# Performance work log

Measured on AMD Instinct MI355X. Metric: run time of the kernel, lower is better.

The kernel has to match this reference:

```python
import jax, jax.numpy as jnp
import numpy as np
from jax import lax


def setup_inputs() -> dict:
    key = jax.random.key(0)
    k1, k2, k3 = jax.random.split(key, 3)
    B, T, dimIn, dimH = 64, 2048, 128, 256
    x = jax.random.normal(k1, (B, T, dimIn), dtype=jnp.float32)
    h = jnp.zeros((B, dimH), dtype=jnp.float32)
    # torch nn.Linear(dimIn+dimH, dimH): weight [dimH, dimIn+dimH], bias [dimH]
    fan_in = dimIn + dimH
    bound = 1.0 / np.sqrt(fan_in)
    W = jax.random.uniform(k2, (dimH, fan_in), minval=-bound, maxval=bound, dtype=jnp.float32)
    b = jax.random.uniform(k3, (dimH,), minval=-bound, maxval=bound, dtype=jnp.float32)
    return {"x": x, "h": h, "W": W, "b": b}


def reference(x, h, W, b):
    # x: [B, T, dimIn], h: [B, H], W: [H, dimIn+H], b: [H]
    dimIn = x.shape[-1]
    Wx = W[:, :dimIn]   # [H, dimIn] -- acts on x part of concat
    Wh = W[:, dimIn:]   # [H, H]     -- acts on h part of concat
    # Precompute the input projection for all timesteps in one GEMM.
    xw = jnp.einsum('btd,hd->bth', x, Wx) + b  # [B, T, H]

    def step(h_prev, xw_t):
        h_new = jnp.tanh(xw_t + h_prev @ Wh.T)  # tanh(Linear(cat(x,h)))
        return h_new, h_new

    _, res = lax.scan(step, h, jnp.swapaxes(xw, 0, 1))  # res: [T, B, H]
    return jnp.swapaxes(res, 0, 1)  # [B, T, H]
```

## Files before the change

kernel.cpp:

```cpp
#include <hip/hip_runtime.h>
#include <hip/hip_fp16.h>

#define TSEQ  2048
#define BATCH 64
#define DIN   128
#define DH    256
#define WSTR  384
#define NCH   (TSEQ / 16)

typedef __fp16 h2    __attribute__((ext_vector_type(2)));
typedef __fp16 f16x8 __attribute__((ext_vector_type(8)));
typedef float  f32x4 __attribute__((ext_vector_type(4)));

static __device__ __forceinline__ h2 bc_h2(unsigned int u) {
    return __builtin_bit_cast(h2, u);
}

#define DPP_XOR1(v) __builtin_bit_cast(float, \
    __builtin_amdgcn_mov_dpp(__builtin_bit_cast(int, (v)), 0xB1, 0xF, 0xF, true))
#define DPP_XOR2(v) __builtin_bit_cast(float, \
    __builtin_amdgcn_mov_dpp(__builtin_bit_cast(int, (v)), 0x4E, 0xF, 0xF, true))
#define DPP_XOR8(v) __builtin_bit_cast(float, \
    __builtin_amdgcn_mov_dpp(__builtin_bit_cast(int, (v)), 0x128, 0xF, 0xF, true))

__global__ __launch_bounds__(256) void xw_gemm(const float* __restrict__ x,
                                               const float* __restrict__ W,
                                               const float* __restrict__ bias,
                                               float* __restrict__ out) {
    __shared__ __align__(16) __fp16 af[64][136];

    const int tid  = threadIdx.x;
    const int lane = tid & 63;
    const int wv   = tid >> 6;
    const int row0 = blockIdx.x * 64;
    const int nlo  = lane & 15;
    const int quad = lane >> 4;

    {
        const int r  = tid >> 2;
        const int c0 = (tid & 3) * 32;
        const float4* xr = (const float4*)(x + (size_t)(row0 + r) * DIN) + (tid & 3) * 8;
#pragma unroll
        for (int i = 0; i < 4; ++i) {
            float4 f0 = xr[2 * i];
            float4 f1 = xr[2 * i + 1];
            f16x8 v;
            v[0]=(__fp16)f0.x; v[1]=(__fp16)f0.y; v[2]=(__fp16)f0.z; v[3]=(__fp16)f0.w;
            v[4]=(__fp16)f1.x; v[5]=(__fp16)f1.y; v[6]=(__fp16)f1.z; v[7]=(__fp16)f1.w;
            *(f16x8*)&af[r][c0 + i * 8] = v;
        }
    }

    f16x8 bfr[4][4];
#pragma unroll
    for (int n0 = 0; n0 < 4; ++n0) {
        const int n = wv * 64 + n0 * 16 + nlo;
        const float* wr = W + (size_t)n * WSTR;
#pragma unroll
        for (int kk = 0; kk < 4; ++kk) {
            const int k = kk * 32 + quad * 8;
            float4 f0 = *(const float4*)(wr + k);
            float4 f1 = *(const float4*)(wr + k + 4);
            f16x8 v;
            v[0]=(__fp16)f0.x; v[1]=(__fp16)f0.y; v[2]=(__fp16)f0.z; v[3]=(__fp16)f0.w;
            v[4]=(__fp16)f1.x; v[5]=(__fp16)f1.y; v[6]=(__fp16)f1.z; v[7]=(__fp16)f1.w;
            bfr[n0][kk] = v;
        }
    }
    __syncthreads();

    f32x4 acc[4][4];
#pragma unroll
    for (int m0 = 0; m0 < 4; ++m0)
#pragma unroll
        for (int n0 = 0; n0 < 4; ++n0) acc[m0][n0] = (f32x4)0.0f;

#pragma unroll
    for (int kk = 0; kk < 4; ++kk) {
#pragma unroll
        for (int m0 = 0; m0 < 4; ++m0) {
            f16x8 a = *(const f16x8*)&af[m0 * 16 + nlo][kk * 32 + quad * 8];
#pragma unroll
            for (int n0 = 0; n0 < 4; ++n0)
                acc[m0][n0] = __builtin_amdgcn_mfma_f32_16x16x32_f16(
                                  a, bfr[n0][kk], acc[m0][n0], 0, 0, 0);
        }
    }

#pragma unroll
    for (int n0 = 0; n0 < 4; ++n0) {
        const int col = wv * 64 + n0 * 16 + nlo;
        const float bn = bias[col];
#pragma unroll
        for (int m0 = 0; m0 < 4; ++m0)
#pragma unroll
            for (int r = 0; r < 4; ++r) {
                const int row = row0 + m0 * 16 + quad * 4 + r;
                out[(size_t)row * DH + col] = acc[m0][n0][r] + bn;
            }
    }
}

__global__ __launch_bounds__(256, 1) void rnn_scan(const float* __restrict__ W,
                                                   const float* __restrict__ h0,
                                                   float* __restrict__ out) {
    __shared__ __align__(16) __fp16 hseg[2][8][40];

    const int tid = threadIdx.x;
    const int b   = blockIdx.x;
    const int sig = (tid & 3) | ((tid & 8) >> 1);

    h2 w[8][16];
#pragma unroll
    for (int r = 0; r < 8; ++r) {
        const int rho = (r & 3) | ((r & 4) << 1);
        const float* wr = W + (size_t)(tid ^ rho) * WSTR + DIN + 32 * sig;
#pragma unroll
        for (int j = 0; j < 8; ++j) {
            float4 f = *(const float4*)(wr + 4 * j);
            w[r][2 * j]     = h2{(__fp16)f.x, (__fp16)f.y};
            w[r][2 * j + 1] = h2{(__fp16)f.z, (__fp16)f.w};
        }
    }
#pragma unroll
    for (int r = 0; r < 8; ++r)
#pragma unroll
        for (int i = 0; i < 16; ++i)
            asm volatile("" : "+v"(w[r][i]));

    hseg[0][tid >> 5][tid & 31] = (__fp16)h0[(size_t)b * DH + tid];

    const float* gsrc = out + (size_t)b * TSEQ * DH + tid;
    float*       gdst = out + (size_t)b * TSEQ * DH + tid;

    float xwreg[16];
#pragma unroll
    for (int s = 0; s < 16; ++s) xwreg[s] = gsrc[(size_t)s * DH];

    asm volatile("s_waitcnt lgkmcnt(0)\n\ts_barrier" ::: "memory");

#pragma unroll 1
    for (int c = 0; c < NCH; ++c) {
        const float* gnext = gsrc + (size_t)(c + 1 < NCH ? c + 1 : 0) * (16 * DH);
        float*       gout  = gdst + (size_t)c * (16 * DH);

#pragma unroll
        for (int s = 0; s < 16; ++s) {
            const float xw_s = xwreg[s];
            xwreg[s] = gnext[(size_t)s * DH];
            const int p = s & 1;
            const uint4* hp = (const uint4*)&hseg[p][sig][0];

            float P[8];
#pragma unroll
            for (int r = 0; r < 8; ++r) P[r] = 0.f;
#pragma unroll
            for (int i4 = 0; i4 < 4; ++i4) {
                uint4 v = hp[i4];
                h2 ha = bc_h2(v.x), hb = bc_h2(v.y), hc = bc_h2(v.z), hd = bc_h2(v.w);
#pragma unroll
                for (int r = 0; r < 8; ++r) {
                    P[r] = __builtin_amdgcn_fdot2(w[r][4*i4+0], ha, P[r], false);
                    P[r] = __builtin_amdgcn_fdot2(w[r][4*i4+1], hb, P[r], false);
                    P[r] = __builtin_amdgcn_fdot2(w[r][4*i4+2], hc, P[r], false);
                    P[r] = __builtin_amdgcn_fdot2(w[r][4*i4+3], hd, P[r], false);
                }
            }

            float S0 = P[0] + DPP_XOR1(P[1]);
            float S1 = P[2] + DPP_XOR1(P[3]);
            float S2 = P[4] + DPP_XOR1(P[5]);
            float S3 = P[6] + DPP_XOR1(P[7]);
            float T0 = S0 + DPP_XOR2(S1);
            float T1 = S2 + DPP_XOR2(S3);
            float dot = T0 + DPP_XOR8(T1);

            float pre = xw_s + dot;
            float e  = __expf(2.0f * pre);
            float hn = 1.0f - 2.0f * __builtin_amdgcn_rcpf(e + 1.0f);

            hseg[p ^ 1][tid >> 5][tid & 31] = (__fp16)hn;
            gout[(size_t)s * DH] = hn;

            asm volatile("s_waitcnt lgkmcnt(0)\n\ts_barrier" ::: "memory");
        }
    }
}

extern "C" void kernel_launch(void* const* d_in, const int* in_sizes, int n_in,
                              void* d_out, int out_size, void* d_ws, size_t ws_size,
                              hipStream_t stream) {
    const float* x    = (const float*)d_in[0];
    const float* h0   = (const float*)d_in[1];
    const float* W    = (const float*)d_in[2];
    const float* bias = (const float*)d_in[3];
    float* out = (float*)d_out;

    xw_gemm<<<BATCH * TSEQ / 64, 256, 0, stream>>>(x, W, bias, out);
    rnn_scan<<<BATCH, 256, 0, stream>>>(W, h0, out);
}
```

Measured before the change: 994.7 us.

## Fuse input projection GEMM into RNN scan and split recurrence over 512 threads

Removes the separate xw GEMM kernel and computes each 16-step chunk of the input projection inside the scan block with MFMA, double-buffered in shared memory and overlapped with the recurrence. Doubles threads per block to 512 so each thread handles half the hidden-state dot product, combining the two halves with a ds_bpermute across lanes 32 apart. This avoids writing xw to global memory and reading it back, and shortens each thread's serial dot-product chain. In exchange each step gains an extra cross-lane reduction and half the threads idle during tanh, and the per-chunk GEMM sits on the scan's critical path.

```diff
diff --git a/kernel.cpp b/kernel.cpp
--- a/kernel.cpp
+++ b/kernel.cpp
@@ -23,100 +23,38 @@
 #define DPP_XOR8(v) __builtin_bit_cast(float, \
     __builtin_amdgcn_mov_dpp(__builtin_bit_cast(int, (v)), 0x128, 0xF, 0xF, true))
 
-__global__ __launch_bounds__(256) void xw_gemm(const float* __restrict__ x,
-                                               const float* __restrict__ W,
-                                               const float* __restrict__ bias,
-                                               float* __restrict__ out) {
-    __shared__ __align__(16) __fp16 af[64][136];
+static __device__ __forceinline__ float pair_sum32(float u, int lane) {
+    const int addr = (lane ^ 32) << 2;
+    float v = __builtin_bit_cast(float,
+        __builtin_amdgcn_ds_bpermute(addr, __builtin_bit_cast(int, u)));
+    return u + v;
+}
+
+__global__ __launch_bounds__(512) void rnn_fused(const float* __restrict__ x,
+                                                 const float* __restrict__ W,
+                                                 const float* __restrict__ bias,
+                                                 const float* __restrict__ h0,
+                                                 float* __restrict__ out) {
+    __shared__ __align__(16) __fp16 hseg[2][16][24];
+    __shared__ __align__(16) float  xwb[2][16][DH];
 
     const int tid  = threadIdx.x;
+    const int b    = blockIdx.x;
     const int lane = tid & 63;
     const int wv   = tid >> 6;
-    const int row0 = blockIdx.x * 64;
     const int nlo  = lane & 15;
     const int quad = lane >> 4;
 
-    {
-        const int r  = tid >> 2;
-        const int c0 = (tid & 3) * 32;
-        const float4* xr = (const float4*)(x + (size_t)(row0 + r) * DIN) + (tid & 3) * 8;
-#pragma unroll
-        for (int i = 0; i < 4; ++i) {
-            float4 f0 = xr[2 * i];
-            float4 f1 = xr[2 * i + 1];
-            f16x8 v;
-            v[0]=(__fp16)f0.x; v[1]=(__fp16)f0.y; v[2]=(__fp16)f0.z; v[3]=(__fp16)f0.w;
-            v[4]=(__fp16)f1.x; v[5]=(__fp16)f1.y; v[6]=(__fp16)f1.z; v[7]=(__fp16)f1.w;
-            *(f16x8*)&af[r][c0 + i * 8] = v;
-        }
-    }
+    const int o   = (tid & 31) | ((tid >> 1) & 224);
+    const int sig = (tid & 3) | ((tid & 8) >> 1) | ((tid & 32) >> 2);
 
-    f16x8 bfr[4][4];
-#pragma unroll
-    for (int n0 = 0; n0 < 4; ++n0) {
-        const int n = wv * 64 + n0 * 16 + nlo;
-        const float* wr = W + (size_t)n * WSTR;
-#pragma unroll
-        for (int kk = 0; kk < 4; ++kk) {
-            const int k = kk * 32 + quad * 8;
-            float4 f0 = *(const float4*)(wr + k);
-            float4 f1 = *(const float4*)(wr + k + 4);
-            f16x8 v;
-            v[0]=(__fp16)f0.x; v[1]=(__fp16)f0.y; v[2]=(__fp16)f0.z; v[3]=(__fp16)f0.w;
-            v[4]=(__fp16)f1.x; v[5]=(__fp16)f1.y; v[6]=(__fp16)f1.z; v[7]=(__fp16)f1.w;
-            bfr[n0][kk] = v;
-        }
-    }
-    __syncthreads();
-
-    f32x4 acc[4][4];
-#pragma unroll
-    for (int m0 = 0; m0 < 4; ++m0)
-#pragma unroll
-        for (int n0 = 0; n0 < 4; ++n0) acc[m0][n0] = (f32x4)0.0f;
-
-#pragma unroll
-    for (int kk = 0; kk < 4; ++kk) {
-#pragma unroll
-        for (int m0 = 0; m0 < 4; ++m0) {
-            f16x8 a = *(const f16x8*)&af[m0 * 16 + nlo][kk * 32 + quad * 8];
-#pragma unroll
-            for (int n0 = 0; n0 < 4; ++n0)
-                acc[m0][n0] = __builtin_amdgcn_mfma_f32_16x16x32_f16(
-                                  a, bfr[n0][kk], acc[m0][n0], 0, 0, 0);
-        }
-    }
-
-#pragma unroll
-    for (int n0 = 0; n0 < 4; ++n0) {
-        const int col = wv * 64 + n0 * 16 + nlo;
-        const float bn = bias[col];
-#pragma unroll
-        for (int m0 = 0; m0 < 4; ++m0)
-#pragma unroll
-            for (int r = 0; r < 4; ++r) {
-                const int row = row0 + m0 * 16 + quad * 4 + r;
-                out[(size_t)row * DH + col] = acc[m0][n0][r] + bn;
-            }
-    }
-}
-
-__global__ __launch_bounds__(256, 1) void rnn_scan(const float* __restrict__ W,
-                                                   const float* __restrict__ h0,
-                                                   float* __restrict__ out) {
-    __shared__ __align__(16) __fp16 hseg[2][8][40];
-
-    const int tid = threadIdx.x;
-    const int b   = blockIdx.x;
-    const int sig = (tid & 3) | ((tid & 8) >> 1);
-
-    h2 w[8][16];
+    h2 w[8][8];
 #pragma unroll
     for (int r = 0; r < 8; ++r) {
         const int rho = (r & 3) | ((r & 4) << 1);
-        const float* wr = W + (size_t)(tid ^ rho) * WSTR + DIN + 32 * sig;
+        const float* wr = W + (size_t)(o ^ rho) * WSTR + DIN + 16 * sig;
 #pragma unroll
-        for (int j = 0; j < 8; ++j) {
+        for (int j = 0; j < 4; ++j) {
             float4 f = *(const float4*)(wr + 4 * j);
             w[r][2 * j]     = h2{(__fp16)f.x, (__fp16)f.y};
             w[r][2 * j + 1] = h2{(__fp16)f.z, (__fp16)f.w};
@@ -125,46 +63,97 @@
 #pragma unroll
     for (int r = 0; r < 8; ++r)
 #pragma unroll
-        for (int i = 0; i < 16; ++i)
+        for (int i = 0; i < 8; ++i)
             asm volatile("" : "+v"(w[r][i]));
 
-    hseg[0][tid >> 5][tid & 31] = (__fp16)h0[(size_t)b * DH + tid];
+    f16x8 bfr[2][4];
+#pragma unroll
+    for (int n0 = 0; n0 < 2; ++n0) {
+        const float* wr = W + (size_t)(32 * wv + 16 * n0 + nlo) * WSTR;
+#pragma unroll
+        for (int kk = 0; kk < 4; ++kk) {
+            float4 f0 = *(const float4*)(wr + kk * 32 + quad * 8);
+            float4 f1 = *(const float4*)(wr + kk * 32 + quad * 8 + 4);
+            f16x8 v;
+            v[0]=(__fp16)f0.x; v[1]=(__fp16)f0.y; v[2]=(__fp16)f0.z; v[3]=(__fp16)f0.w;
+            v[4]=(__fp16)f1.x; v[5]=(__fp16)f1.y; v[6]=(__fp16)f1.z; v[7]=(__fp16)f1.w;
+            bfr[n0][kk] = v;
+        }
+    }
+    const float bias0 = bias[32 * wv + nlo];
+    const float bias1 = bias[32 * wv + 16 + nlo];
 
-    const float* gsrc = out + (size_t)b * TSEQ * DH + tid;
-    float*       gdst = out + (size_t)b * TSEQ * DH + tid;
+    const float* xb = x + (size_t)b * TSEQ * DIN;
+    float4 xr[8];
 
-    float xwreg[16];
-#pragma unroll
-    for (int s = 0; s < 16; ++s) xwreg[s] = gsrc[(size_t)s * DH];
+#define LOAD_X(c)                                                            \
+    {                                                                        \
+        const float* xp = xb + (size_t)(16 * (c) + nlo) * DIN;               \
+        _Pragma("unroll")                                                    \
+        for (int kk = 0; kk < 4; ++kk) {                                     \
+            xr[2 * kk]     = *(const float4*)(xp + kk * 32 + quad * 8);      \
+            xr[2 * kk + 1] = *(const float4*)(xp + kk * 32 + quad * 8 + 4);  \
+        }                                                                    \
+    }
 
-    asm volatile("s_waitcnt lgkmcnt(0)\n\ts_barrier" ::: "memory");
+#define MAKE_XW(buf)                                                         \
+    {                                                                        \
+        f32x4 a0 = (f32x4)0.0f, a1 = (f32x4)0.0f;                            \
+        _Pragma("unroll")                                                    \
+        for (int kk = 0; kk < 4; ++kk) {                                     \
+            float4 f0 = xr[2 * kk], f1 = xr[2 * kk + 1];                     \
+            f16x8 a;                                                         \
+            a[0]=(__fp16)f0.x; a[1]=(__fp16)f0.y; a[2]=(__fp16)f0.z;         \
+            a[3]=(__fp16)f0.w; a[4]=(__fp16)f1.x; a[5]=(__fp16)f1.y;         \
+            a[6]=(__fp16)f1.z; a[7]=(__fp16)f1.w;                            \
+            a0 = __builtin_amdgcn_mfma_f32_16x16x32_f16(a, bfr[0][kk], a0, 0, 0, 0); \
+            a1 = __builtin_amdgcn_mfma_f32_16x16x32_f16(a, bfr[1][kk], a1, 0, 0, 0); \
+        }                                                                    \
+        _Pragma("unroll")                                                    \
+        for (int r = 0; r < 4; ++r) {                                        \
+            xwb[buf][quad * 4 + r][32 * wv + nlo]      = a0[r] + bias0;      \
+            xwb[buf][quad * 4 + r][32 * wv + 16 + nlo] = a1[r] + bias1;      \
+        }                                                                    \
+    }
+
+    if (tid < DH) hseg[0][tid >> 4][tid & 15] = (__fp16)h0[(size_t)b * DH + tid];
+
+    LOAD_X(0);
+    MAKE_XW(0);
+    LOAD_X(1);
+    __syncthreads();
+
+    float* orow = out + (size_t)b * TSEQ * DH + o;
 
 #pragma unroll 1
     for (int c = 0; c < NCH; ++c) {
-        const float* gnext = gsrc + (size_t)(c + 1 < NCH ? c + 1 : 0) * (16 * DH);
-        float*       gout  = gdst + (size_t)c * (16 * DH);
+        if (c + 1 < NCH) {
+            MAKE_XW((c + 1) & 1);
+            LOAD_X(c + 2 < NCH ? c + 2 : 0);
+        }
+        const float* xwr = &xwb[c & 1][0][0];
+        float* oc = orow + (size_t)(16 * c) * DH;
 
 #pragma unroll
         for (int s = 0; s < 16; ++s) {
-            const float xw_s = xwreg[s];
-            xwreg[s] = gnext[(size_t)s * DH];
+            const float xw_s = xwr[s * DH + o];
             const int p = s & 1;
             const uint4* hp = (const uint4*)&hseg[p][sig][0];
+            uint4 v0 = hp[0], v1 = hp[1];
+            h2 ha = bc_h2(v0.x), hb = bc_h2(v0.y), hc = bc_h2(v0.z), hd = bc_h2(v0.w);
+            h2 he = bc_h2(v1.x), hf = bc_h2(v1.y), hg = bc_h2(v1.z), hh = bc_h2(v1.w);
 
             float P[8];
 #pragma unroll
-            for (int r = 0; r < 8; ++r) P[r] = 0.f;
-#pragma unroll
-            for (int i4 = 0; i4 < 4; ++i4) {
-                uint4 v = hp[i4];
-                h2 ha = bc_h2(v.x), hb = bc_h2(v.y), hc = bc_h2(v.z), hd = bc_h2(v.w);
-#pragma unroll
-                for (int r = 0; r < 8; ++r) {
-                    P[r] = __builtin_amdgcn_fdot2(w[r][4*i4+0], ha, P[r], false);
-                    P[r] = __builtin_amdgcn_fdot2(w[r][4*i4+1], hb, P[r], false);
-                    P[r] = __builtin_amdgcn_fdot2(w[r][4*i4+2], hc, P[r], false);
-                    P[r] = __builtin_amdgcn_fdot2(w[r][4*i4+3], hd, P[r], false);
-                }
+            for (int r = 0; r < 8; ++r) {
+                P[r] = __builtin_amdgcn_fdot2(w[r][0], ha, 0.0f, false);
+                P[r] = __builtin_amdgcn_fdot2(w[r][1], hb, P[r], false);
+                P[r] = __builtin_amdgcn_fdot2(w[r][2], hc, P[r], false);
+                P[r] = __builtin_amdgcn_fdot2(w[r][3], hd, P[r], false);
+                P[r] = __builtin_amdgcn_fdot2(w[r][4], he, P[r], false);
+                P[r] = __builtin_amdgcn_fdot2(w[r][5], hf, P[r], false);
+                P[r] = __builtin_amdgcn_fdot2(w[r][6], hg, P[r], false);
+                P[r] = __builtin_amdgcn_fdot2(w[r][7], hh, P[r], false);
             }
 
             float S0 = P[0] + DPP_XOR1(P[1]);
@@ -173,18 +162,21 @@
             float S3 = P[6] + DPP_XOR1(P[7]);
             float T0 = S0 + DPP_XOR2(S1);
             float T1 = S2 + DPP_XOR2(S3);
-            float dot = T0 + DPP_XOR8(T1);
+            float U  = T0 + DPP_XOR8(T1);
+            float dot = pair_sum32(U, lane);
 
-            float pre = xw_s + dot;
-            float e  = __expf(2.0f * pre);
-            float hn = 1.0f - 2.0f * __builtin_amdgcn_rcpf(e + 1.0f);
-
-            hseg[p ^ 1][tid >> 5][tid & 31] = (__fp16)hn;
-            gout[(size_t)s * DH] = hn;
-
+            if (!(tid & 32)) {
+                float pre = xw_s + dot;
+                float e  = __expf(2.0f * pre);
+                float hn = 1.0f - 2.0f * __builtin_amdgcn_rcpf(e + 1.0f);
+                hseg[p ^ 1][o >> 4][o & 15] = (__fp16)hn;
+                oc[(size_t)s * DH] = hn;
+            }
             asm volatile("s_waitcnt lgkmcnt(0)\n\ts_barrier" ::: "memory");
         }
     }
+#undef LOAD_X
+#undef MAKE_XW
 }
 
 extern "C" void kernel_launch(void* const* d_in, const int* in_sizes, int n_in,
@@ -196,6 +188,5 @@
     const float* bias = (const float*)d_in[3];
     float* out = (float*)d_out;
 
-    xw_gemm<<<BATCH * TSEQ / 64, 256, 0, stream>>>(x, W, bias, out);
-    rnn_scan<<<BATCH, 256, 0, stream>>>(W, h0, out);
+    rnn_fused<<<BATCH, 512, 0, stream>>>(x, W, bias, h0, out);
 }
```

After: 1.188 ms. +19.4%, slower.
